# Optimization experiments

Hardware: AMD Instinct MI355X
Metric: run time of the kernel (lower is better)

The kernel has to match this reference:

```python
import jax, jax.numpy as jnp
import numpy as np

B = 4096      # graphs
N = 21        # nodes per graph (EEG electrodes)
CIN = 512
H1 = 1024
H2 = 1024
COUT = 512
R = 4         # SE reduction
RANK = 10     # nodevec rank
EPS = 1e-5
THRESH = 0.1


def setup_inputs() -> dict:
    key = jax.random.key(0)
    ks = jax.random.split(key, 16)
    p = lambda i, shape, s=0.02: (jax.random.normal(ks[i], shape, jnp.float32) * s)
    return {
        "x": jax.random.normal(ks[0], (B * N, CIN), jnp.float32),
        "batch": jnp.arange(B * N, dtype=jnp.int32) // N,
        "nodevec1": jax.random.normal(ks[1], (N, RANK), jnp.float32),
        "nodevec2": jax.random.normal(ks[2], (RANK, N), jnp.float32),
        "se_w1": p(3, (CIN, CIN // R), 0.05),
        "se_w2": p(4, (CIN // R, CIN), 0.05),
        "W1": p(5, (CIN, H1)), "b1": jnp.zeros((H1,), jnp.float32),
        "W2": p(6, (H1, H2)), "b2": jnp.zeros((H2,), jnp.float32),
        "W3": p(7, (H2, COUT)), "b3": jnp.zeros((COUT,), jnp.float32),
        "bn1_g": jnp.ones((H1,), jnp.float32), "bn1_b": jnp.zeros((H1,), jnp.float32),
        "bn2_g": jnp.ones((H2,), jnp.float32), "bn2_b": jnp.zeros((H2,), jnp.float32),
        "bn3_g": jnp.ones((COUT,), jnp.float32), "bn3_b": jnp.zeros((COUT,), jnp.float32),
        "rs1_w": p(8, (CIN, H1)), "rs1_b": jnp.zeros((H1,), jnp.float32),
        "fc_w": p(9, (COUT, 2 * COUT)), "fc_b": jnp.zeros((2 * COUT,), jnp.float32),
    }


def _batchnorm(h, g, b):
    # training-mode BN: biased batch stats over the node dimension
    m = h.mean(0)
    v = h.var(0)
    return (h - m) * jax.lax.rsqrt(v + EPS) * g + b


def _gcn(A, h, W, b):
    # GCNConv with precomputed normalized+thresholded weights:
    # out = A_block_diag @ (h @ W) + b, done densely per graph since A is 21x21
    hm = (h @ W).reshape(B, N, -1)                 # [B, N, Cout]
    agg = jnp.einsum('ij,bjc->bic', A, hm)         # message passing per graph
    return agg.reshape(B * N, -1) + b


def _forward(x, batch, nodevec1, nodevec2, se_w1, se_w2,
             W1, b1, W2, b2, W3, b3,
             bn1_g, bn1_b, bn2_g, bn2_b, bn3_g, bn3_b,
             rs1_w, rs1_b, fc_w, fc_b):
    # SE layer on [B, N, C]: channel-wise gating from node-mean features
    x3 = x.reshape(B, N, CIN)
    y = jax.nn.sigmoid(jax.nn.relu(x3.mean(1) @ se_w1) @ se_w2)   # [B, C]
    xg = (x3 * y[:, None, :]).reshape(B * N, CIN)
    # adaptive adjacency: sigmoid(nv1 @ nv2), symmetric normalize, threshold
    adp = jax.nn.sigmoid(nodevec1 @ nodevec2)                      # [N, N]
    at = adp + jnp.eye(N, dtype=adp.dtype)
    deg = at.sum(1)
    dinv = jnp.where(deg > 0, deg ** -0.5, 0.0)
    A = dinv[:, None] * at * dinv[None, :]
    A = jnp.where(A > THRESH, A, 0.0)
    # layer 1 (+ projected residual, BN, relu; dropout omitted = eval)
    h = _batchnorm(_gcn(A, xg, W1, b1), bn1_g, bn1_b) + (xg @ rs1_w + rs1_b)
    h = jax.nn.relu(h)
    # layer 2 (h1 == h2 -> identity residual)
    h = jax.nn.relu(_batchnorm(_gcn(A, h, W2, b2), bn2_g, bn2_b) + h)
    # layer 3
    h = _batchnorm(_gcn(A, h, W3, b3), bn3_g, bn3_b)
    # global mean pool by graph id
    ssum = jax.ops.segment_sum(h, batch, num_segments=B)
    cnt = jax.ops.segment_sum(jnp.ones((h.shape[0], 1), h.dtype), batch, num_segments=B)
    pooled = ssum / cnt
    return pooled @ fc_w + fc_b                                    # [B, 2*COUT]


def reference(x, batch, nodevec1, nodevec2, se_w1, se_w2,
              W1, b1, W2, b2, W3, b3,
              bn1_g, bn1_b, bn2_g, bn2_b, bn3_g, bn3_b,
              rs1_w, rs1_b, fc_w, fc_b):
    return _forward(x, batch, nodevec1, nodevec2, se_w1, se_w2,
                    W1, b1, W2, b2, W3, b3,
                    bn1_g, bn1_b, bn2_g, bn2_b, bn3_g, bn3_b,
                    rs1_w, rs1_b, fc_w, fc_b)
```

## Files before the change

### kernel.cpp

```cpp
#include <hip/hip_runtime.h>

typedef _Float16 f16;
typedef f16 f16x2 __attribute__((ext_vector_type(2)));
typedef f16 f16x4 __attribute__((ext_vector_type(4)));
typedef f16 f16x8 __attribute__((ext_vector_type(8)));
typedef float f32x4 __attribute__((ext_vector_type(4)));
typedef const void __attribute__((address_space(1)))* gas1;
typedef void __attribute__((address_space(3)))* las3;

#define NB 4096
#define NN 21
#define MROWS (NB*NN)
#define CIN 512

__global__ void k_adj(const float* __restrict__ nv1, const float* __restrict__ nv2,
                      float* __restrict__ Aout) {
  __shared__ float at[21][21];
  __shared__ float dinv[21];
  int t = threadIdx.x;
  if (t < 441) {
    int i = t / 21, j = t % 21;
    float s = 0.f;
    #pragma unroll
    for (int r = 0; r < 10; r++) s += nv1[i*10 + r] * nv2[r*21 + j];
    float v = 1.f / (1.f + expf(-s));
    if (i == j) v += 1.f;
    at[i][j] = v;
  }
  __syncthreads();
  if (t < 21) {
    float d = 0.f;
    #pragma unroll
    for (int j = 0; j < 21; j++) d += at[t][j];
    dinv[t] = d > 0.f ? rsqrtf(d) : 0.f;
  }
  __syncthreads();
  if (t < 441) {
    int i = t / 21, j = t % 21;
    float a = dinv[i] * at[i][j] * dinv[j];
    Aout[t] = a > 0.1f ? a : 0.f;
  }
}

__global__ void k_transpose(const float* __restrict__ src, f16* __restrict__ dst,
                            int K, int N) {
  __shared__ float tile[32][33];
  int n0 = blockIdx.x * 32, k0 = blockIdx.y * 32;
  int tx = threadIdx.x, ty = threadIdx.y;
  #pragma unroll
  for (int i = 0; i < 4; i++)
    tile[ty + 8*i][tx] = src[(size_t)(k0 + ty + 8*i) * N + n0 + tx];
  __syncthreads();
  #pragma unroll
  for (int i = 0; i < 4; i++)
    dst[(size_t)(n0 + ty + 8*i) * K + k0 + tx] = (f16)tile[tx][ty + 8*i];
}

__global__ void k_mean(const float* __restrict__ x, float* __restrict__ xm) {
  int b = blockIdx.x, t = threadIdx.x;
  for (int c = t; c < CIN; c += 256) {
    float s = 0.f;
    #pragma unroll
    for (int n = 0; n < NN; n++) s += x[((size_t)b*NN + n)*CIN + c];
    xm[(size_t)b*CIN + c] = s * (1.f/21.f);
  }
}

__global__ void k_se1(const float* __restrict__ xm, const float* __restrict__ w1,
                      float* __restrict__ y1) {
  __shared__ float row[CIN];
  int b = blockIdx.x, t = threadIdx.x;
  for (int k = t; k < CIN; k += 128) row[k] = xm[(size_t)b*CIN + k];
  __syncthreads();
  float acc = 0.f;
  for (int k = 0; k < CIN; k++) acc += row[k] * w1[(size_t)k*128 + t];
  y1[(size_t)b*128 + t] = fmaxf(acc, 0.f);
}

__global__ void k_se2(const float* __restrict__ y1, const float* __restrict__ w2,
                      float* __restrict__ y) {
  __shared__ float row[128];
  int b = blockIdx.x, t = threadIdx.x;
  if (t < 128) row[t] = y1[(size_t)b*128 + t];
  __syncthreads();
  float acc = 0.f;
  for (int k = 0; k < 128; k++) acc += row[k] * w2[(size_t)k*CIN + t];
  y[(size_t)b*CIN + t] = 1.f / (1.f + expf(-acc));
}

__global__ void k_gate(const float* __restrict__ x, const float* __restrict__ y,
                       f16* __restrict__ xg) {
  size_t i8 = (size_t)blockIdx.x * 256 + threadIdx.x;
  size_t base = i8 * 8;
  int r = (int)(base >> 9);
  int c = (int)(base & 511);
  int b = r / 21;
  const float4* xp = (const float4*)(x + base);
  const float4* yp = (const float4*)(y + (size_t)b*CIN + c);
  float4 a0 = xp[0], a1 = xp[1];
  float4 g0 = yp[0], g1 = yp[1];
  f16x8 o;
  o[0] = (f16)(a0.x * g0.x); o[1] = (f16)(a0.y * g0.y);
  o[2] = (f16)(a0.z * g0.z); o[3] = (f16)(a0.w * g0.w);
  o[4] = (f16)(a1.x * g1.x); o[5] = (f16)(a1.y * g1.y);
  o[6] = (f16)(a1.z * g1.z); o[7] = (f16)(a1.w * g1.w);
  *(f16x8*)(xg + base) = o;
}

#define QBUF 65536

template<int MODE>
__global__ __launch_bounds__(512, 1)
void k_gemm256(const f16* __restrict__ A, const f16* __restrict__ BT,
               f16* __restrict__ C1, const float* __restrict__ bias,
               float* __restrict__ Cf, float* __restrict__ psum,
               float* __restrict__ psq, int N, int K, int lgn) {
  __shared__ __align__(16) char lds[2 * QBUF];
  const int tid = threadIdx.x;
  const int nwg = gridDim.x;
  const int g = blockIdx.x;
  const int swz = (g & 7) * (nwg >> 3) + (g >> 3);
  const int bn = swz & ((1 << lgn) - 1);
  const int bm = swz >> lgn;
  const int lane = tid & 63;
  const int wid = tid >> 6;
  const int wr = wid >> 2;
  const int wc = wid & 3;
  const int fr = lane & 15;
  const int kg = lane >> 4;

  int srcOff[8];
  #pragma unroll
  for (int j = 0; j < 8; j++) {
    int gid = j * 512 + tid;
    int row = (gid >> 3) & 255;
    int gr = gid & 7;
    int gsw = gr ^ (row & 7);
    srcOff[j] = ((j < 4 ? bm : bn) * 256 + row) * K + gsw * 8;
  }
  const int ldsBase = tid * 16;

  const int x7 = fr & 7;
  const int aBase = (wr*128 + fr) * 128;
  const int bBase = 32768 + (wc*64 + fr) * 128;

  f32x4 acc[8][4];
  #pragma unroll
  for (int m = 0; m < 8; m++)
    #pragma unroll
    for (int n = 0; n < 4; n++)
      #pragma unroll
      for (int r = 0; r < 4; r++) acc[m][n][r] = 0.f;

  auto STAGE2 = [&](int t2, int sbuf, int j0) {
    char* dst = (char*)lds + sbuf * QBUF;
    const size_t kof = (size_t)t2 * 64;
    #pragma unroll
    for (int j = j0; j < j0 + 2; j++) {
      const f16* src = (j < 4 ? A : BT) + srcOff[j] + kof;
      __builtin_amdgcn_global_load_lds((gas1)src, (las3)(dst + ldsBase + j*8192), 16, 0, 0);
    }
  };
  auto READB = [&](f16x8* bv, const char* rb, int s) {
    const int ko = ((s*4 + kg) ^ x7) << 4;
    #pragma unroll
    for (int n = 0; n < 4; n++) bv[n] = *(const f16x8*)(rb + bBase + n*2048 + ko);
  };
  auto READA4 = [&](f16x8* av, const char* rb, int s, int mh) {
    const int ko = ((s*4 + kg) ^ x7) << 4;
    #pragma unroll
    for (int mi = 0; mi < 4; mi++)
      av[mi] = *(const f16x8*)(rb + aBase + (mh*4 + mi)*2048 + ko);
  };

  const int NT = K >> 6;
  STAGE2(0, 0, 0); STAGE2(0, 0, 2); STAGE2(0, 0, 4); STAGE2(0, 0, 6);
  asm volatile("s_waitcnt vmcnt(0)" ::: "memory");
  asm volatile("s_barrier" ::: "memory");

  for (int t = 0; t < NT; t++) {
    const char* rb = (const char*)lds + (t & 1) * QBUF;
    const int nb = (t + 1) & 1;
    const bool stg = (t + 1) < NT;
    f16x8 av[4], bv[4];

    READB(bv, rb, 0); READA4(av, rb, 0, 0);
    if (stg) STAGE2(t + 1, nb, 0);
    __builtin_amdgcn_s_setprio(1);
    #pragma unroll
    for (int mi = 0; mi < 4; mi++)
      #pragma unroll
      for (int n = 0; n < 4; n++)
        acc[mi][n] = __builtin_amdgcn_mfma_f32_16x16x32_f16(bv[n], av[mi], acc[mi][n], 0, 0, 0);
    __builtin_amdgcn_s_setprio(0);
    __builtin_amdgcn_sched_barrier(0);

    READA4(av, rb, 0, 1);
    if (stg) STAGE2(t + 1, nb, 2);
    __builtin_amdgcn_s_setprio(1);
    #pragma unroll
    for (int mi = 0; mi < 4; mi++)
      #pragma unroll
      for (int n = 0; n < 4; n++)
        acc[4 + mi][n] = __builtin_amdgcn_mfma_f32_16x16x32_f16(bv[n], av[mi], acc[4 + mi][n], 0, 0, 0);
    __builtin_amdgcn_s_setprio(0);
    __builtin_amdgcn_sched_barrier(0);

    READB(bv, rb, 1); READA4(av, rb, 1, 0);
    if (stg) STAGE2(t + 1, nb, 4);
    __builtin_amdgcn_s_setprio(1);
    #pragma unroll
    for (int mi = 0; mi < 4; mi++)
      #pragma unroll
      for (int n = 0; n < 4; n++)
        acc[mi][n] = __builtin_amdgcn_mfma_f32_16x16x32_f16(bv[n], av[mi], acc[mi][n], 0, 0, 0);
    __builtin_amdgcn_s_setprio(0);
    __builtin_amdgcn_sched_barrier(0);

    READA4(av, rb, 1, 1);
    if (stg) STAGE2(t + 1, nb, 6);
    __builtin_amdgcn_s_setprio(1);
    #pragma unroll
    for (int mi = 0; mi < 4; mi++)
      #pragma unroll
      for (int n = 0; n < 4; n++)
        acc[4 + mi][n] = __builtin_amdgcn_mfma_f32_16x16x32_f16(bv[n], av[mi], acc[4 + mi][n], 0, 0, 0);
    __builtin_amdgcn_s_setprio(0);
    __builtin_amdgcn_sched_barrier(0);

    if (stg) {
      asm volatile("s_waitcnt vmcnt(0)" ::: "memory");
      asm volatile("s_barrier" ::: "memory");
    }
  }

  const int crow = bm*256 + wr*128 + fr;
  const int ccol = bn*256 + wc*64 + kg*4;
  if constexpr (MODE == 2) {
    #pragma unroll
    for (int n = 0; n < 4; n++) {
      float4 bb = *(const float4*)(bias + ccol + n*16);
      #pragma unroll
      for (int m = 0; m < 8; m++) {
        float4 v;
        v.x = acc[m][n][0] + bb.x; v.y = acc[m][n][1] + bb.y;
        v.z = acc[m][n][2] + bb.z; v.w = acc[m][n][3] + bb.w;
        *(float4*)(Cf + (size_t)(crow + m*16) * N + ccol + n*16) = v;
      }
    }
  } else {
    #pragma unroll
    for (int m = 0; m < 8; m++)
      #pragma unroll
      for (int n = 0; n < 4; n++) {
        f16x4 o;
        o[0] = (f16)acc[m][n][0]; o[1] = (f16)acc[m][n][1];
        o[2] = (f16)acc[m][n][2]; o[3] = (f16)acc[m][n][3];
        *(f16x4*)(C1 + (size_t)(crow + m*16) * N + ccol + n*16) = o;
      }
  }
  if constexpr (MODE == 1) {
    float s[4][4], q[4][4];
    #pragma unroll
    for (int n = 0; n < 4; n++)
      #pragma unroll
      for (int r = 0; r < 4; r++) {
        float ss = 0.f, qq = 0.f;
        #pragma unroll
        for (int m = 0; m < 8; m++) { float v = acc[m][n][r]; ss += v; qq = fmaf(v, v, qq); }
        s[n][r] = ss; q[n][r] = qq;
      }
    #pragma unroll
    for (int n = 0; n < 4; n++)
      #pragma unroll
      for (int r = 0; r < 4; r++) {
        s[n][r] += __shfl_xor(s[n][r], 1); s[n][r] += __shfl_xor(s[n][r], 2);
        s[n][r] += __shfl_xor(s[n][r], 4); s[n][r] += __shfl_xor(s[n][r], 8);
        q[n][r] += __shfl_xor(q[n][r], 1); q[n][r] += __shfl_xor(q[n][r], 2);
        q[n][r] += __shfl_xor(q[n][r], 4); q[n][r] += __shfl_xor(q[n][r], 8);
      }
    float* wred = (float*)lds;
    __syncthreads();
    if (fr == 0) {
      #pragma unroll
      for (int n = 0; n < 4; n++)
        #pragma unroll
        for (int r = 0; r < 4; r++) {
          int c = wc*64 + n*16 + kg*4 + r;
          wred[wr*256 + c]       = s[n][r];
          wred[512 + wr*256 + c] = q[n][r];
        }
    }
    __syncthreads();
    if (tid < 256) {
      psum[(size_t)bm * N + bn*256 + tid] = wred[tid]       + wred[256 + tid];
      psq [(size_t)bm * N + bn*256 + tid] = wred[512 + tid] + wred[768 + tid];
    }
  }
}

__global__ __launch_bounds__(256)
void k_mixip(f16* __restrict__ t, const float* __restrict__ Aadj) {
  __shared__ float A[441];
  int b = blockIdx.x, tid = threadIdx.x;
  for (int i = tid; i < 441; i += 256) A[i] = Aadj[i];
  __syncthreads();
  int c0 = tid * 2;
  size_t base = (size_t)b * NN * 512 + c0;
  float vx[21], vy[21];
  #pragma unroll
  for (int j = 0; j < 21; j++) {
    f16x2 v = *(const f16x2*)(t + base + (size_t)j * 512);
    vx[j] = (float)v[0]; vy[j] = (float)v[1];
  }
  #pragma unroll
  for (int i = 0; i < 21; i++) {
    float a0 = 0.f, a1 = 0.f;
    #pragma unroll
    for (int j = 0; j < 21; j++) { float w = A[i*21+j]; a0 = fmaf(w, vx[j], a0); a1 = fmaf(w, vy[j], a1); }
    f16x2 o; o[0] = (f16)a0; o[1] = (f16)a1;
    *(f16x2*)(t + base + (size_t)i * 512) = o;
  }
}

__global__ __launch_bounds__(256)
void k_mix(f16* __restrict__ t, const float* __restrict__ Aadj,
           float* __restrict__ psum, float* __restrict__ psq, int C) {
  __shared__ float A[441];
  int b = blockIdx.x, tid = threadIdx.x;
  for (int i = tid; i < 441; i += 256) A[i] = Aadj[i];
  __syncthreads();
  int c0 = (blockIdx.y * 256 + tid) * 2;
  size_t base = (size_t)b * NN * C + c0;
  float vx[21], vy[21];
  #pragma unroll
  for (int j = 0; j < 21; j++) {
    f16x2 v = *(const f16x2*)(t + base + (size_t)j * C);
    vx[j] = (float)v[0]; vy[j] = (float)v[1];
  }
  float s0 = 0.f, s1 = 0.f, q0 = 0.f, q1 = 0.f;
  #pragma unroll
  for (int i = 0; i < 21; i++) {
    float a0 = 0.f, a1 = 0.f;
    #pragma unroll
    for (int j = 0; j < 21; j++) {
      float w = A[i*21 + j];
      a0 = fmaf(w, vx[j], a0);
      a1 = fmaf(w, vy[j], a1);
    }
    f16x2 o; o[0] = (f16)a0; o[1] = (f16)a1;
    *(f16x2*)(t + base + (size_t)i * C) = o;
    s0 += a0; s1 += a1;
    q0 = fmaf(a0, a0, q0); q1 = fmaf(a1, a1, q1);
  }
  float2 sv; sv.x = s0; sv.y = s1;
  float2 qv; qv.x = q0; qv.y = q1;
  *(float2*)(psum + (size_t)b * C + c0) = sv;
  *(float2*)(psq  + (size_t)b * C + c0) = qv;
}

__global__ void k_reduce(const float* __restrict__ ps, const float* __restrict__ pq,
                         float* __restrict__ rs, float* __restrict__ rq,
                         int C, int per) {
  int c = blockIdx.x * 256 + threadIdx.x;
  int py = blockIdx.y;
  float s = 0.f, q = 0.f;
  for (int p = py*per; p < py*per + per; p++) {
    s += ps[(size_t)p*C + c];
    q += pq[(size_t)p*C + c];
  }
  rs[(size_t)py*C + c] = s;
  rq[(size_t)py*C + c] = q;
}

__global__ void k_bnparams(const float* __restrict__ psum, const float* __restrict__ psq,
                           const float* __restrict__ gamma, const float* __restrict__ beta,
                           const float* __restrict__ resbias,
                           float* __restrict__ scale, float* __restrict__ shift,
                           int C, int npart) {
  int c = blockIdx.x * 256 + threadIdx.x;
  float s = 0.f, q = 0.f;
  for (int p = 0; p < npart; p++) { s += psum[(size_t)p*C + c]; q += psq[(size_t)p*C + c]; }
  const float Minv = 1.f / (float)MROWS;
  float mean = s * Minv;
  float var = q * Minv - mean * mean;
  float sc = gamma[c] * rsqrtf(var + 1e-5f);
  float sh = beta[c] - mean * sc;
  if (resbias) sh += resbias[c];
  scale[c] = sc; shift[c] = sh;
}

__global__ void k_finalize(const f16* __restrict__ g, const f16* res,
                           f16* dst, const float* __restrict__ scale,
                           const float* __restrict__ shift, int cmask) {
  size_t i8 = (size_t)blockIdx.x * 256 + threadIdx.x;
  size_t base = i8 * 8;
  int c = (int)(base & (size_t)cmask);
  f16x8 gv = *(const f16x8*)(g + base);
  f16x8 rv = *(const f16x8*)(res + base);
  f16x8 o;
  #pragma unroll
  for (int j = 0; j < 8; j++) {
    float v = (float)gv[j] * scale[c + j] + shift[c + j] + (float)rv[j];
    o[j] = (f16)fmaxf(v, 0.f);
  }
  *(f16x8*)(dst + base) = o;
}

__global__ __launch_bounds__(256)
void k_finmix(const f16* t, const f16* res, f16* hout, f16* hmix,
              const float* __restrict__ scale, const float* __restrict__ shift,
              const float* __restrict__ Aadj, int C) {
  __shared__ float A[441];
  int b = blockIdx.x, tid = threadIdx.x;
  for (int i = tid; i < 441; i += 256) A[i] = Aadj[i];
  __syncthreads();
  int c0 = (blockIdx.y * 256 + tid) * 2;
  float scx = scale[c0], scy = scale[c0+1];
  float shx = shift[c0], shy = shift[c0+1];
  size_t base = (size_t)b * NN * C + c0;
  float hx[21], hy[21];
  #pragma unroll
  for (int j = 0; j < 21; j++) {
    f16x2 tv = *(const f16x2*)(t + base + (size_t)j*C);
    f16x2 rv = *(const f16x2*)(res + base + (size_t)j*C);
    hx[j] = fmaxf((float)tv[0]*scx + shx + (float)rv[0], 0.f);
    hy[j] = fmaxf((float)tv[1]*scy + shy + (float)rv[1], 0.f);
    if (hout) {
      f16x2 o; o[0] = (f16)hx[j]; o[1] = (f16)hy[j];
      *(f16x2*)(hout + base + (size_t)j*C) = o;
    }
  }
  #pragma unroll
  for (int i = 0; i < 21; i++) {
    float a0 = 0.f, a1 = 0.f;
    #pragma unroll
    for (int j = 0; j < 21; j++) { float w = A[i*21+j]; a0 = fmaf(w, hx[j], a0); a1 = fmaf(w, hy[j], a1); }
    f16x2 o; o[0] = (f16)a0; o[1] = (f16)a1;
    *(f16x2*)(hmix + base + (size_t)i*C) = o;
  }
}

__global__ void k_pool(const f16* __restrict__ g3, const float* __restrict__ scale,
                       const float* __restrict__ shift, f16* __restrict__ pooled) {
  int b = blockIdx.x, t = threadIdx.x;
  for (int c = t; c < 512; c += 256) {
    float s = 0.f;
    #pragma unroll
    for (int n = 0; n < NN; n++) s += (float)g3[((size_t)b*NN + n)*512 + c];
    pooled[(size_t)b*512 + c] = (f16)((s * (1.f/21.f)) * scale[c] + shift[c]);
  }
}

extern "C" void kernel_launch(void* const* d_in, const int* in_sizes, int n_in,
                              void* d_out, int out_size, void* d_ws, size_t ws_size,
                              hipStream_t stream) {
  const float* x     = (const float*)d_in[0];
  const float* nv1   = (const float*)d_in[2];
  const float* nv2   = (const float*)d_in[3];
  const float* se_w1 = (const float*)d_in[4];
  const float* se_w2 = (const float*)d_in[5];
  const float* W1    = (const float*)d_in[6];
  const float* W2    = (const float*)d_in[8];
  const float* W3    = (const float*)d_in[10];
  const float* bn1g  = (const float*)d_in[12];
  const float* bn1b  = (const float*)d_in[13];
  const float* bn2g  = (const float*)d_in[14];
  const float* bn2b  = (const float*)d_in[15];
  const float* bn3g  = (const float*)d_in[16];
  const float* bn3b  = (const float*)d_in[17];
  const float* rs1w  = (const float*)d_in[18];
  const float* rs1b  = (const float*)d_in[19];
  const float* fcw   = (const float*)d_in[20];
  const float* fcb   = (const float*)d_in[21];
  float* out = (float*)d_out;

  char* ws = (char*)d_ws;
  size_t off = 0;
  auto alloc = [&](size_t bytes) -> char* {
    char* p = ws + off;
    off = (off + bytes + 255) & ~(size_t)255;
    return p;
  };

  float* A_adj = (float*)alloc(441 * 4);
  f16* W1T  = (f16*)alloc((size_t)1024 * 512 * 2);
  f16* RS1T = (f16*)alloc((size_t)1024 * 512 * 2);
  f16* W2T  = (f16*)alloc((size_t)1024 * 1024 * 2);
  f16* W3T  = (f16*)alloc((size_t)512 * 1024 * 2);
  f16* FCWT = (f16*)alloc((size_t)1024 * 512 * 2);
  float* psum = (float*)alloc((size_t)NB * 1024 * 4);
  float* psq  = (float*)alloc((size_t)NB * 1024 * 4);
  float* y1   = (float*)alloc((size_t)NB * 128 * 4);
  float* rsum = (float*)alloc((size_t)32 * 1024 * 4);
  float* rsq  = (float*)alloc((size_t)32 * 1024 * 4);
  float* sc1 = (float*)alloc(1024 * 4);
  float* sh1 = (float*)alloc(1024 * 4);
  float* sc2 = (float*)alloc(1024 * 4);
  float* sh2 = (float*)alloc(1024 * 4);
  float* sc3 = (float*)alloc(1024 * 4);
  float* sh3 = (float*)alloc(1024 * 4);
  f16* pooled = (f16*)alloc((size_t)NB * 512 * 2);
  f16* G = (f16*)alloc((size_t)MROWS * 512 * 2);
  f16* R = (f16*)alloc((size_t)MROWS * 1024 * 2);
  f16* T = (f16*)alloc((size_t)MROWS * 1024 * 2);
  float* xm = psum;
  float* yv = psq;
  (void)ws_size; (void)in_sizes; (void)n_in; (void)out_size;

  k_adj<<<1, 512, 0, stream>>>(nv1, nv2, A_adj);
  k_transpose<<<dim3(32, 16), dim3(32, 8), 0, stream>>>(W1,   W1T,  512, 1024);
  k_transpose<<<dim3(32, 16), dim3(32, 8), 0, stream>>>(rs1w, RS1T, 512, 1024);
  k_transpose<<<dim3(32, 32), dim3(32, 8), 0, stream>>>(W2,   W2T,  1024, 1024);
  k_transpose<<<dim3(16, 32), dim3(32, 8), 0, stream>>>(W3,   W3T,  1024, 512);
  k_transpose<<<dim3(32, 16), dim3(32, 8), 0, stream>>>(fcw,  FCWT, 512, 1024);

  k_mean<<<NB, 256, 0, stream>>>(x, xm);
  k_se1<<<NB, 128, 0, stream>>>(xm, se_w1, y1);
  k_se2<<<NB, 512, 0, stream>>>(y1, se_w2, yv);
  k_gate<<<21504, 256, 0, stream>>>(x, yv, G);

  k_gemm256<0><<<1344, 512, 0, stream>>>(G, RS1T, R, nullptr, nullptr, nullptr, nullptr, 1024, 512, 2);
  k_mixip<<<NB, 256, 0, stream>>>(G, A_adj);
  k_gemm256<1><<<1344, 512, 0, stream>>>(G, W1T, T, nullptr, nullptr, psum, psq, 1024, 512, 2);
  k_reduce<<<dim3(4, 24), 256, 0, stream>>>(psum, psq, rsum, rsq, 1024, 14);
  k_bnparams<<<4, 256, 0, stream>>>(rsum, rsq, bn1g, bn1b, rs1b, sc1, sh1, 1024, 24);
  k_finalize<<<43008, 256, 0, stream>>>(T, R, R, sc1, sh1, 1023);

  k_gemm256<0><<<1344, 512, 0, stream>>>(R, W2T, T, nullptr, nullptr, nullptr, nullptr, 1024, 1024, 2);
  k_mix<<<dim3(NB, 2), 256, 0, stream>>>(T, A_adj, psum, psq, 1024);
  k_reduce<<<dim3(4, 32), 256, 0, stream>>>(psum, psq, rsum, rsq, 1024, 128);
  k_bnparams<<<4, 256, 0, stream>>>(rsum, rsq, bn2g, bn2b, nullptr, sc2, sh2, 1024, 32);
  k_finmix<<<dim3(NB, 2), 256, 0, stream>>>(T, R, nullptr, T, sc2, sh2, A_adj, 1024);

  k_gemm256<1><<<672, 512, 0, stream>>>(T, W3T, G, nullptr, nullptr, psum, psq, 512, 1024, 1);
  k_reduce<<<dim3(2, 24), 256, 0, stream>>>(psum, psq, rsum, rsq, 512, 14);
  k_bnparams<<<2, 256, 0, stream>>>(rsum, rsq, bn3g, bn3b, nullptr, sc3, sh3, 512, 24);

  k_pool<<<NB, 256, 0, stream>>>(G, sc3, sh3, pooled);
  k_gemm256<2><<<64, 512, 0, stream>>>(pooled, FCWT, nullptr, fcb, out, nullptr, nullptr, 1024, 512, 2);
}
```

Baseline: 1.188 ms.

## Deepen GEMM prefetch to half-tile granularity and merge weight transposes

Reorganizes the GEMM LDS layout into two 32-wide k-halves with a new XOR swizzle, and prefetches the first half of tile t+2 while tile t is being consumed. Partial vmcnt waits and a mid-iteration barrier replace the full drain, so global loads stay in flight across tile boundaries instead of stalling each iteration. The five weight-transpose launches are also folded into one kernel to cut launch overhead. The risks are extra barriers per iteration and the correctness of the new swizzle and wait counts.

```diff
diff --git a/kernel.cpp b/kernel.cpp
--- a/kernel.cpp
+++ b/kernel.cpp
@@ -42,10 +42,22 @@
   }
 }
 
-__global__ void k_transpose(const float* __restrict__ src, f16* __restrict__ dst,
-                            int K, int N) {
+__global__ void k_transpose_all(const float* __restrict__ s0, const float* __restrict__ s1,
+                                const float* __restrict__ s2, const float* __restrict__ s3,
+                                const float* __restrict__ s4,
+                                f16* __restrict__ d0, f16* __restrict__ d1,
+                                f16* __restrict__ d2, f16* __restrict__ d3,
+                                f16* __restrict__ d4) {
   __shared__ float tile[32][33];
-  int n0 = blockIdx.x * 32, k0 = blockIdx.y * 32;
+  int b = blockIdx.x;
+  const float* src; f16* dst; int K, N, local;
+  if (b < 512)       { src = s0; dst = d0; K = 512;  N = 1024; local = b; }
+  else if (b < 1024) { src = s1; dst = d1; K = 512;  N = 1024; local = b - 512; }
+  else if (b < 2048) { src = s2; dst = d2; K = 1024; N = 1024; local = b - 1024; }
+  else if (b < 2560) { src = s3; dst = d3; K = 1024; N = 512;  local = b - 2048; }
+  else               { src = s4; dst = d4; K = 512;  N = 1024; local = b - 2560; }
+  int ntn = N >> 5;
+  int n0 = (local % ntn) * 32, k0 = (local / ntn) * 32;
   int tx = threadIdx.x, ty = threadIdx.y;
   #pragma unroll
   for (int i = 0; i < 4; i++)
@@ -129,20 +141,29 @@
   const int fr = lane & 15;
   const int kg = lane >> 4;
 
-  int srcOff[8];
+  int srcOff[8]; int ldsOff[8];
   #pragma unroll
   for (int j = 0; j < 8; j++) {
-    int gid = j * 512 + tid;
-    int row = (gid >> 3) & 255;
-    int gr = gid & 7;
-    int gsw = gr ^ (row & 7);
-    srcOff[j] = ((j < 4 ? bm : bn) * 256 + row) * K + gsw * 8;
-  }
-  const int ldsBase = tid * 16;
-
-  const int x7 = fr & 7;
-  const int aBase = (wr*128 + fr) * 128;
-  const int bBase = 32768 + (wc*64 + fr) * 128;
+    int s = j >> 2, mat = (j >> 1) & 1, jj = j & 1;
+    int idx = jj * 512 + tid;
+    int row = idx >> 2;
+    int gr  = tid & 3;
+    int gsw = gr ^ ((row ^ (row >> 2)) & 3);
+    srcOff[j] = ((mat ? bn : bm) * 256 + row) * K + s*32 + gsw*8;
+    ldsOff[j] = s*32768 + mat*16384 + idx*16;
+  }
+
+  int aOff[8], axor[8], bOff[4], bxor[4];
+  #pragma unroll
+  for (int m = 0; m < 8; m++) {
+    int row = wr*128 + m*16 + fr;
+    aOff[m] = row * 64; axor[m] = (row ^ (row >> 2)) & 3;
+  }
+  #pragma unroll
+  for (int n = 0; n < 4; n++) {
+    int row = wc*64 + n*16 + fr;
+    bOff[n] = 16384 + row * 64; bxor[n] = (row ^ (row >> 2)) & 3;
+  }
 
   f32x4 acc[8][4];
   #pragma unroll
@@ -157,35 +178,38 @@
     const size_t kof = (size_t)t2 * 64;
     #pragma unroll
     for (int j = j0; j < j0 + 2; j++) {
-      const f16* src = (j < 4 ? A : BT) + srcOff[j] + kof;
-      __builtin_amdgcn_global_load_lds((gas1)src, (las3)(dst + ldsBase + j*8192), 16, 0, 0);
+      const f16* src = (((j >> 1) & 1) ? BT : A) + srcOff[j] + kof;
+      __builtin_amdgcn_global_load_lds((gas1)src, (las3)(dst + ldsOff[j]), 16, 0, 0);
     }
   };
   auto READB = [&](f16x8* bv, const char* rb, int s) {
-    const int ko = ((s*4 + kg) ^ x7) << 4;
-    #pragma unroll
-    for (int n = 0; n < 4; n++) bv[n] = *(const f16x8*)(rb + bBase + n*2048 + ko);
+    #pragma unroll
+    for (int n = 0; n < 4; n++)
+      bv[n] = *(const f16x8*)(rb + s*32768 + bOff[n] + ((kg ^ bxor[n]) << 4));
   };
   auto READA4 = [&](f16x8* av, const char* rb, int s, int mh) {
-    const int ko = ((s*4 + kg) ^ x7) << 4;
     #pragma unroll
     for (int mi = 0; mi < 4; mi++)
-      av[mi] = *(const f16x8*)(rb + aBase + (mh*4 + mi)*2048 + ko);
+      av[mi] = *(const f16x8*)(rb + s*32768 + aOff[mh*4 + mi] + ((kg ^ axor[mh*4 + mi]) << 4));
   };
 
   const int NT = K >> 6;
-  STAGE2(0, 0, 0); STAGE2(0, 0, 2); STAGE2(0, 0, 4); STAGE2(0, 0, 6);
-  asm volatile("s_waitcnt vmcnt(0)" ::: "memory");
+  STAGE2(0, 0, 0); STAGE2(0, 0, 2);
+  STAGE2(0, 0, 4); STAGE2(0, 0, 6);
+  STAGE2(1, 1, 0); STAGE2(1, 1, 2);
+  asm volatile("s_waitcnt vmcnt(8)" ::: "memory");
   asm volatile("s_barrier" ::: "memory");
 
   for (int t = 0; t < NT; t++) {
     const char* rb = (const char*)lds + (t & 1) * QBUF;
-    const int nb = (t + 1) & 1;
-    const bool stg = (t + 1) < NT;
+    const int nb  = (t + 1) & 1;
+    const int nb2 = t & 1;
+    const bool s1 = (t + 1) < NT;
+    const bool s2 = (t + 2) < NT;
     f16x8 av[4], bv[4];
 
     READB(bv, rb, 0); READA4(av, rb, 0, 0);
-    if (stg) STAGE2(t + 1, nb, 0);
+    if (s1) STAGE2(t + 1, nb, 4);
     __builtin_amdgcn_s_setprio(1);
     #pragma unroll
     for (int mi = 0; mi < 4; mi++)
@@ -196,7 +220,7 @@
     __builtin_amdgcn_sched_barrier(0);
 
     READA4(av, rb, 0, 1);
-    if (stg) STAGE2(t + 1, nb, 2);
+    if (s1) STAGE2(t + 1, nb, 6);
     __builtin_amdgcn_s_setprio(1);
     #pragma unroll
     for (int mi = 0; mi < 4; mi++)
@@ -206,8 +230,12 @@
     __builtin_amdgcn_s_setprio(0);
     __builtin_amdgcn_sched_barrier(0);
 
+    if (s1) asm volatile("s_waitcnt vmcnt(8)" ::: "memory");
+    else    asm volatile("s_waitcnt vmcnt(0)" ::: "memory");
+    asm volatile("s_barrier" ::: "memory");
+
     READB(bv, rb, 1); READA4(av, rb, 1, 0);
-    if (stg) STAGE2(t + 1, nb, 4);
+    if (s2) STAGE2(t + 2, nb2, 0);
     __builtin_amdgcn_s_setprio(1);
     #pragma unroll
     for (int mi = 0; mi < 4; mi++)
@@ -218,7 +246,7 @@
     __builtin_amdgcn_sched_barrier(0);
 
     READA4(av, rb, 1, 1);
-    if (stg) STAGE2(t + 1, nb, 6);
+    if (s2) STAGE2(t + 2, nb2, 2);
     __builtin_amdgcn_s_setprio(1);
     #pragma unroll
     for (int mi = 0; mi < 4; mi++)
@@ -228,8 +256,9 @@
     __builtin_amdgcn_s_setprio(0);
     __builtin_amdgcn_sched_barrier(0);
 
-    if (stg) {
-      asm volatile("s_waitcnt vmcnt(0)" ::: "memory");
+    if (s1) {
+      if (s2) asm volatile("s_waitcnt vmcnt(8)" ::: "memory");
+      else    asm volatile("s_waitcnt vmcnt(4)" ::: "memory");
       asm volatile("s_barrier" ::: "memory");
     }
   }
@@ -509,11 +538,8 @@
   (void)ws_size; (void)in_sizes; (void)n_in; (void)out_size;
 
   k_adj<<<1, 512, 0, stream>>>(nv1, nv2, A_adj);
-  k_transpose<<<dim3(32, 16), dim3(32, 8), 0, stream>>>(W1,   W1T,  512, 1024);
-  k_transpose<<<dim3(32, 16), dim3(32, 8), 0, stream>>>(rs1w, RS1T, 512, 1024);
-  k_transpose<<<dim3(32, 32), dim3(32, 8), 0, stream>>>(W2,   W2T,  1024, 1024);
-  k_transpose<<<dim3(16, 32), dim3(32, 8), 0, stream>>>(W3,   W3T,  1024, 512);
-  k_transpose<<<dim3(32, 16), dim3(32, 8), 0, stream>>>(fcw,  FCWT, 512, 1024);
+  k_transpose_all<<<3072, dim3(32, 8), 0, stream>>>(W1, rs1w, W2, W3, fcw,
+                                                    W1T, RS1T, W2T, W3T, FCWT);
 
   k_mean<<<NB, 256, 0, stream>>>(x, xm);
   k_se1<<<NB, 128, 0, stream>>>(xm, se_w1, y1);
```

Measured after the change: 1.198 ms. Within noise of the previous version (+0.9%).
